# Performance work log

Measured on AMD Instinct MI355X. Metric: run time of the kernel, lower is better.

Reference implementation:

```python
import jax, jax.numpy as jnp
import numpy as np

B, T, N, IN_DIM = 32, 12, 1024, 1
HID, EMB, K, HOR, OUT = 64, 16, 2, 12, 1


def setup_inputs() -> dict:
    key = jax.random.key(0)
    ks = jax.random.split(key, 12)
    s = 0.1
    return {
        "x": jax.random.normal(ks[0], (B, T, N, IN_DIM), jnp.float32),
        "E": jax.random.normal(ks[1], (N, EMB), jnp.float32),
        # layer 1: gate (z,r) and candidate pools; in = IN_DIM + HID
        "Wg1": jax.random.normal(ks[2], (EMB, K, IN_DIM + HID, 2 * HID), jnp.float32) * s,
        "bg1": jax.random.normal(ks[3], (EMB, 2 * HID), jnp.float32) * s,
        "Wc1": jax.random.normal(ks[4], (EMB, K, IN_DIM + HID, HID), jnp.float32) * s,
        "bc1": jax.random.normal(ks[5], (EMB, HID), jnp.float32) * s,
        # layer 2: in = HID + HID
        "Wg2": jax.random.normal(ks[6], (EMB, K, 2 * HID, 2 * HID), jnp.float32) * s,
        "bg2": jax.random.normal(ks[7], (EMB, 2 * HID), jnp.float32) * s,
        "Wc2": jax.random.normal(ks[8], (EMB, K, 2 * HID, HID), jnp.float32) * s,
        "bc2": jax.random.normal(ks[9], (EMB, HID), jnp.float32) * s,
        # Conv2d(1, HOR*OUT, kernel=(1, HID)) == per-node linear HID -> HOR*OUT
        "Wout": jax.random.normal(ks[10], (HOR * OUT, HID), jnp.float32) * s,
        "bout": jnp.zeros((HOR * OUT,), jnp.float32),
    }


def _supports(E):
    # adaptive adjacency from node embeddings + Chebyshev polynomial set
    A = jax.nn.softmax(jax.nn.relu(E @ E.T), axis=1)  # [N, N]
    sup = [jnp.eye(E.shape[0], dtype=E.dtype), A]
    for _ in range(K - 2):
        sup.append(2.0 * (A @ sup[-1]) - sup[-2])
    return jnp.stack(sup[:K])  # [K, N, N]


def _gconv(x, sup, E, Wp, bp):
    # x: [B, N, Ci]; per-node weights generated from embeddings
    xg = jnp.einsum('knm,bmc->bnkc', sup, x)          # [B, N, K, Ci]
    W = jnp.einsum('nd,dkio->nkio', E, Wp)            # [N, K, Ci, Co]
    b = E @ bp                                        # [N, Co]
    return jnp.einsum('bnki,nkio->bno', xg, W) + b


def _layer(xs, sup, E, Wg, bg, Wc, bc):
    # xs: [T, B, N, Ci]; adaptive graph-conv GRU scanned over time
    hid = Wc.shape[-1]

    def step(h, x_t):
        zr = jax.nn.sigmoid(_gconv(jnp.concatenate([x_t, h], -1), sup, E, Wg, bg))
        z, r = jnp.split(zr, 2, axis=-1)
        hc = jnp.tanh(_gconv(jnp.concatenate([x_t, z * h], -1), sup, E, Wc, bc))
        h_new = r * h + (1.0 - r) * hc
        return h_new, h_new

    h0 = jnp.zeros((xs.shape[1], xs.shape[2], hid), xs.dtype)
    _, hs = jax.lax.scan(step, h0, xs)
    return hs  # [T, B, N, hid]


def reference(x, E, Wg1, bg1, Wc1, bc1, Wg2, bg2, Wc2, bc2, Wout, bout):
    sup = _supports(E)
    xs = jnp.swapaxes(x, 0, 1)                        # [T, B, N, in]
    h1 = _layer(xs, sup, E, Wg1, bg1, Wc1, bc1)       # [T, B, N, HID]
    h2 = _layer(h1, sup, E, Wg2, bg2, Wc2, bc2)       # [T, B, N, HID]
    h_last = h2[-1]                                   # [B, N, HID]
    out = jnp.einsum('bnh,oh->bno', h_last, Wout) + bout  # [B, N, HOR*OUT]
    out = jnp.transpose(out, (0, 2, 1)).reshape(x.shape[0], HOR, OUT, N)
    return jnp.transpose(out, (0, 1, 3, 2))           # [B, HOR, N, OUT]
```

## Files before the change

kernel.cpp:

```cpp
#include <hip/hip_runtime.h>
#include <math.h>

#define NN 1024
#define BB 32
#define TTT 12
#define HH 64
#define DD 16

__device__ __forceinline__ float dot4f(const float4 v, const float* __restrict__ wv) {
    return v.x * wv[0] + v.y * wv[1] + v.z * wv[2] + v.w * wv[3];
}

__device__ __forceinline__ float sigmoidf_(float x) { return 1.0f / (1.0f + expf(-x)); }

__global__ __launch_bounds__(256) void compute_A_kernel(const float* __restrict__ E,
                                                        float* __restrict__ A) {
    int n = blockIdx.x;
    int tid = threadIdx.x;
    __shared__ float en[DD];
    __shared__ float red[256];
    if (tid < DD) en[tid] = E[n * DD + tid];
    __syncthreads();
    float s[4];
    float lmax = 0.0f;
    #pragma unroll
    for (int it = 0; it < 4; ++it) {
        int m = tid + it * 256;
        float acc = 0.0f;
        #pragma unroll
        for (int d = 0; d < DD; ++d) acc += en[d] * E[m * DD + d];
        acc = fmaxf(acc, 0.0f);
        s[it] = acc;
        lmax = fmaxf(lmax, acc);
    }
    red[tid] = lmax; __syncthreads();
    for (int st = 128; st > 0; st >>= 1) {
        if (tid < st) red[tid] = fmaxf(red[tid], red[tid + st]);
        __syncthreads();
    }
    float mx = red[0];
    __syncthreads();
    float lsum = 0.0f;
    #pragma unroll
    for (int it = 0; it < 4; ++it) { s[it] = expf(s[it] - mx); lsum += s[it]; }
    red[tid] = lsum; __syncthreads();
    for (int st = 128; st > 0; st >>= 1) {
        if (tid < st) red[tid] += red[tid + st];
        __syncthreads();
    }
    float inv = 1.0f / red[0];
    #pragma unroll
    for (int it = 0; it < 4; ++it) {
        int m = tid + it * 256;
        A[n * NN + m] = s[it] * inv;
    }
}

__global__ __launch_bounds__(256) void gen_w_f32_kernel(const float* __restrict__ E,
                                                        const float* __restrict__ Wp,
                                                        float* __restrict__ out,
                                                        int rowlen, int total) {
    int idx = blockIdx.x * 256 + threadIdx.x;
    if (idx >= total) return;
    int n = idx / rowlen;
    int j = idx - n * rowlen;
    const float* e = E + n * DD;
    float acc = 0.0f;
    #pragma unroll
    for (int d = 0; d < DD; ++d) acc += e[d] * Wp[d * rowlen + j];
    out[idx] = acc;
}

__global__ __launch_bounds__(256) void gen_w4_kernel(const float* __restrict__ E,
                                                     const float4* __restrict__ Wp4,
                                                     float4* __restrict__ out4,
                                                     int rowlen4, int total4) {
    int idx = blockIdx.x * 256 + threadIdx.x;
    if (idx >= total4) return;
    int n = idx / rowlen4;
    int j = idx - n * rowlen4;
    const float* e = E + n * DD;
    float4 acc = make_float4(0.f, 0.f, 0.f, 0.f);
    #pragma unroll
    for (int d = 0; d < DD; ++d) {
        float ed = e[d];
        float4 w = Wp4[(size_t)d * rowlen4 + j];
        acc.x += ed * w.x; acc.y += ed * w.y; acc.z += ed * w.z; acc.w += ed * w.w;
    }
    out4[idx] = acc;
}

__global__ __launch_bounds__(256) void transpose_x_kernel(const float* __restrict__ x,
                                                          float* __restrict__ xTm) {
    int idx = blockIdx.x * 256 + threadIdx.x;
    int m = idx / (TTT * BB);
    int tb = idx - m * (TTT * BB);
    int t = tb >> 5;
    int b = tb & 31;
    xTm[idx] = x[(b * TTT + t) * NN + m];
}

__global__ __launch_bounds__(256) void diffuse_gemm(const float* __restrict__ A,
                                                    const float* __restrict__ S,
                                                    float* __restrict__ C, int cols) {
    __shared__ alignas(16) float As[2][16][68];
    __shared__ alignas(16) float Bs[2][16][64];
    const int tid = threadIdx.x;
    const int tx = tid & 15, ty = tid >> 4;
    const int rowbase = blockIdx.y * 64, colbase = blockIdx.x * 64;
    const int kl = tid & 15, r0 = (tid >> 4) * 4;
    const int ml = tid >> 6, cl = tid & 63;
    float pa[4], pb[4];
    #pragma unroll
    for (int r = 0; r < 4; ++r)
        pa[r] = A[(size_t)(rowbase + r0 + r) * NN + kl];
    #pragma unroll
    for (int mm = 0; mm < 4; ++mm)
        pb[mm] = S[(size_t)(ml + mm * 4) * cols + colbase + cl];
    #pragma unroll
    for (int r = 0; r < 4; ++r) As[0][kl][r0 + r] = pa[r];
    #pragma unroll
    for (int mm = 0; mm < 4; ++mm) Bs[0][ml + mm * 4][cl] = pb[mm];
    __syncthreads();
    int cur = 0;
    float acc[4][4] = {};
    for (int kt = 0; kt < NN; kt += 16) {
        int kn = kt + 16;
        if (kn < NN) {
            #pragma unroll
            for (int r = 0; r < 4; ++r)
                pa[r] = A[(size_t)(rowbase + r0 + r) * NN + kn + kl];
            #pragma unroll
            for (int mm = 0; mm < 4; ++mm)
                pb[mm] = S[(size_t)(kn + ml + mm * 4) * cols + colbase + cl];
        }
        #pragma unroll
        for (int kk = 0; kk < 16; ++kk) {
            float4 a = *(const float4*)&As[cur][kk][ty * 4];
            float4 b = *(const float4*)&Bs[cur][kk][tx * 4];
            acc[0][0] += a.x * b.x; acc[0][1] += a.x * b.y; acc[0][2] += a.x * b.z; acc[0][3] += a.x * b.w;
            acc[1][0] += a.y * b.x; acc[1][1] += a.y * b.y; acc[1][2] += a.y * b.z; acc[1][3] += a.y * b.w;
            acc[2][0] += a.z * b.x; acc[2][1] += a.z * b.y; acc[2][2] += a.z * b.z; acc[2][3] += a.z * b.w;
            acc[3][0] += a.w * b.x; acc[3][1] += a.w * b.y; acc[3][2] += a.w * b.z; acc[3][3] += a.w * b.w;
        }
        if (kn < NN) {
            int nxt = cur ^ 1;
            #pragma unroll
            for (int r = 0; r < 4; ++r) As[nxt][kl][r0 + r] = pa[r];
            #pragma unroll
            for (int mm = 0; mm < 4; ++mm) Bs[nxt][ml + mm * 4][cl] = pb[mm];
            __syncthreads();
            cur = nxt;
        }
    }
    #pragma unroll
    for (int i = 0; i < 4; ++i) {
        float4 v = make_float4(acc[i][0], acc[i][1], acc[i][2], acc[i][3]);
        *(float4*)&C[(size_t)(rowbase + ty * 4 + i) * cols + colbase + tx * 4] = v;
    }
}


__global__ __launch_bounds__(256) void l1_gate_kernel(int t,
        const float* __restrict__ xTm, const float* __restrict__ AxA,
        const float* __restrict__ h1, const float* __restrict__ Ah1,
        const float* __restrict__ Wg, const float* __restrict__ Bg,
        float* __restrict__ zh, float* __restrict__ rb) {
    int n = blockIdx.x;
    int tid = threadIdx.x;
    __shared__ alignas(16) float sh[BB * HH];
    __shared__ alignas(16) float sa[BB * HH];
    __shared__ float sx[BB], sax[BB];
    for (int i = tid; i < BB * HH; i += 256) {
        sh[i] = h1[(size_t)n * (BB * HH) + i];
        sa[i] = Ah1[(size_t)n * (BB * HH) + i];
    }
    if (tid < BB) sx[tid] = xTm[n * (TTT * BB) + t * BB + tid];
    else if (tid < 2 * BB) sax[tid - BB] = AxA[n * (TTT * BB) + t * BB + (tid - BB)];
    __syncthreads();
    const int o = tid & 63;
    const int bq = tid >> 6;
    const float* W = Wg + (size_t)n * 16640;
    float accA[8], accB[8];
    float biasA = Bg[n * 128 + o], biasB = Bg[n * 128 + 64 + o];
    float wxa0 = W[o], wxa1 = W[8320 + o];
    float wxb0 = W[64 + o], wxb1 = W[8320 + 64 + o];
    #pragma unroll
    for (int j = 0; j < 8; ++j) {
        int b = bq * 8 + j;
        accA[j] = biasA + sx[b] * wxa0 + sax[b] * wxa1;
        accB[j] = biasB + sx[b] * wxb0 + sax[b] * wxb1;
    }
    for (int i = 0; i < HH; i += 4) {
        float w0a[4], w1a[4], w0b[4], w1b[4];
        #pragma unroll
        for (int q = 0; q < 4; ++q) {
            int row = (1 + i + q) * 128;
            w0a[q] = W[row + o];            w1a[q] = W[8320 + row + o];
            w0b[q] = W[row + 64 + o];       w1b[q] = W[8320 + row + 64 + o];
        }
        #pragma unroll
        for (int j = 0; j < 8; ++j) {
            int b = bq * 8 + j;
            float4 hv = *(const float4*)&sh[b * HH + i];
            float4 av = *(const float4*)&sa[b * HH + i];
            accA[j] += dot4f(hv, w0a) + dot4f(av, w1a);
            accB[j] += dot4f(hv, w0b) + dot4f(av, w1b);
        }
    }
    #pragma unroll
    for (int j = 0; j < 8; ++j) {
        int b = bq * 8 + j;
        float z = sigmoidf_(accA[j]);
        float r = sigmoidf_(accB[j]);
        zh[(size_t)n * (BB * HH) + b * HH + o] = z * sh[b * HH + o];
        rb[(size_t)n * (BB * HH) + b * HH + o] = r;
    }
}

__global__ __launch_bounds__(256) void l1_cand_kernel(int t,
        const float* __restrict__ xTm, const float* __restrict__ AxA,
        const float* __restrict__ zhb, const float* __restrict__ azh,
        const float* __restrict__ Wc, const float* __restrict__ Bc,
        const float* __restrict__ rb, float* __restrict__ h1) {
    int n = blockIdx.x;
    int tid = threadIdx.x;
    __shared__ alignas(16) float sz[BB * HH];
    __shared__ alignas(16) float saz[BB * HH];
    __shared__ float sx[BB], sax[BB];
    for (int i = tid; i < BB * HH; i += 256) {
        sz[i] = zhb[(size_t)n * (BB * HH) + i];
        saz[i] = azh[(size_t)n * (BB * HH) + i];
    }
    if (tid < BB) sx[tid] = xTm[n * (TTT * BB) + t * BB + tid];
    else if (tid < 2 * BB) sax[tid - BB] = AxA[n * (TTT * BB) + t * BB + (tid - BB)];
    __syncthreads();
    const int o = tid & 63;
    const int bq = tid >> 6;
    const float* W = Wc + (size_t)n * 8320;
    float acc[8];
    float bias = Bc[n * 64 + o];
    float wx0 = W[o], wx1 = W[4160 + o];
    #pragma unroll
    for (int j = 0; j < 8; ++j) {
        int b = bq * 8 + j;
        acc[j] = bias + sx[b] * wx0 + sax[b] * wx1;
    }
    for (int i = 0; i < HH; i += 4) {
        float w0[4], w1[4];
        #pragma unroll
        for (int q = 0; q < 4; ++q) {
            int row = (1 + i + q) * 64;
            w0[q] = W[row + o];
            w1[q] = W[4160 + row + o];
        }
        #pragma unroll
        for (int j = 0; j < 8; ++j) {
            int b = bq * 8 + j;
            float4 zv = *(const float4*)&sz[b * HH + i];
            float4 av = *(const float4*)&saz[b * HH + i];
            acc[j] += dot4f(zv, w0) + dot4f(av, w1);
        }
    }
    #pragma unroll
    for (int j = 0; j < 8; ++j) {
        int b = bq * 8 + j;
        size_t idx = (size_t)n * (BB * HH) + b * HH + o;
        float hc = tanhf(acc[j]);
        float r = rb[idx];
        float hold = h1[idx];
        h1[idx] = r * hold + (1.0f - r) * hc;
    }
}


__global__ __launch_bounds__(256) void l2_gate_fused(
        const float* __restrict__ h1, const float* __restrict__ Ah1,
        const float* __restrict__ h2, const float* __restrict__ Ah2,
        const float* __restrict__ E, const float4* __restrict__ Wp4,
        const float* __restrict__ Bg,
        float* __restrict__ zh, float* __restrict__ rb) {
    int n = blockIdx.x, tid = threadIdx.x;
    __shared__ float en[DD];
    __shared__ alignas(16) float Wl[64 * 128];
    __shared__ alignas(16) float Sl[4][BB * HH];
    if (tid < DD) en[tid] = E[n * DD + tid];
    for (int i = tid; i < BB * HH; i += 256) {
        size_t base = (size_t)n * (BB * HH) + i;
        Sl[0][i] = h1[base]; Sl[1][i] = h2[base];
        Sl[2][i] = Ah1[base]; Sl[3][i] = Ah2[base];
    }
    __syncthreads();
    const int o = tid & 63, bq = tid >> 6;
    float accA[8], accB[8];
    float biasA = Bg[n * 128 + o], biasB = Bg[n * 128 + 64 + o];
    #pragma unroll
    for (int j = 0; j < 8; ++j) { accA[j] = biasA; accB[j] = biasB; }
    for (int p = 0; p < 4; ++p) {
        int k = p >> 1, half = p & 1;
        for (int idx = tid; idx < 2048; idx += 256) {
            float4 a = make_float4(0.f, 0.f, 0.f, 0.f);
            #pragma unroll
            for (int d = 0; d < DD; ++d) {
                float ed = en[d];
                float4 w = Wp4[(size_t)d * 8192 + k * 4096 + half * 2048 + idx];
                a.x += ed * w.x; a.y += ed * w.y; a.z += ed * w.z; a.w += ed * w.w;
            }
            *(float4*)&Wl[idx * 4] = a;
        }
        __syncthreads();
        const float* S = Sl[k * 2 + half];
        for (int i = 0; i < HH; i += 4) {
            float wa[4], wb[4];
            #pragma unroll
            for (int q = 0; q < 4; ++q) {
                int row = (i + q) * 128;
                wa[q] = Wl[row + o]; wb[q] = Wl[row + 64 + o];
            }
            #pragma unroll
            for (int j = 0; j < 8; ++j) {
                int b = bq * 8 + j;
                float4 sv = *(const float4*)&S[b * HH + i];
                accA[j] += dot4f(sv, wa); accB[j] += dot4f(sv, wb);
            }
        }
        __syncthreads();
    }
    #pragma unroll
    for (int j = 0; j < 8; ++j) {
        int b = bq * 8 + j;
        float z = sigmoidf_(accA[j]);
        float r = sigmoidf_(accB[j]);
        zh[(size_t)n * (BB * HH) + b * HH + o] = z * Sl[1][b * HH + o];
        rb[(size_t)n * (BB * HH) + b * HH + o] = r;
    }
}

__global__ __launch_bounds__(256) void l2_cand_fused(
        const float* __restrict__ h1, const float* __restrict__ Ah1,
        const float* __restrict__ zhb, const float* __restrict__ azh,
        const float* __restrict__ E, const float4* __restrict__ Wp4,
        const float* __restrict__ Bc,
        const float* __restrict__ rb, float* __restrict__ h2) {
    int n = blockIdx.x, tid = threadIdx.x;
    __shared__ float en[DD];
    __shared__ alignas(16) float Wl[64 * 64];
    __shared__ alignas(16) float Sl[4][BB * HH];
    if (tid < DD) en[tid] = E[n * DD + tid];
    for (int i = tid; i < BB * HH; i += 256) {
        size_t base = (size_t)n * (BB * HH) + i;
        Sl[0][i] = h1[base];  Sl[1][i] = zhb[base];
        Sl[2][i] = Ah1[base]; Sl[3][i] = azh[base];
    }
    __syncthreads();
    const int o = tid & 63, bq = tid >> 6;
    float acc[8];
    float bias = Bc[n * 64 + o];
    #pragma unroll
    for (int j = 0; j < 8; ++j) acc[j] = bias;
    for (int p = 0; p < 4; ++p) {
        int k = p >> 1, half = p & 1;
        for (int idx = tid; idx < 1024; idx += 256) {
            float4 a = make_float4(0.f, 0.f, 0.f, 0.f);
            #pragma unroll
            for (int d = 0; d < DD; ++d) {
                float ed = en[d];
                float4 w = Wp4[(size_t)d * 4096 + k * 2048 + half * 1024 + idx];
                a.x += ed * w.x; a.y += ed * w.y; a.z += ed * w.z; a.w += ed * w.w;
            }
            *(float4*)&Wl[idx * 4] = a;
        }
        __syncthreads();
        const float* S = Sl[k * 2 + half];
        for (int i = 0; i < HH; i += 4) {
            float wa[4];
            #pragma unroll
            for (int qq = 0; qq < 4; ++qq) wa[qq] = Wl[(i + qq) * 64 + o];
            #pragma unroll
            for (int j = 0; j < 8; ++j) {
                int b = bq * 8 + j;
                float4 sv = *(const float4*)&S[b * HH + i];
                acc[j] += dot4f(sv, wa);
            }
        }
        __syncthreads();
    }
    #pragma unroll
    for (int j = 0; j < 8; ++j) {
        int b = bq * 8 + j;
        size_t idx = (size_t)n * (BB * HH) + b * HH + o;
        float hc = tanhf(acc[j]);
        float r = rb[idx];
        float hold = h2[idx];
        h2[idx] = r * hold + (1.0f - r) * hc;
    }
}

__global__ __launch_bounds__(384) void out_kernel(const float* __restrict__ h2,
                                                  const float* __restrict__ Wout,
                                                  const float* __restrict__ bout,
                                                  float* __restrict__ out) {
    int n = blockIdx.x;
    int tid = threadIdx.x;
    __shared__ float shh[BB * HH];
    __shared__ float sw[TTT * HH];
    __shared__ float sb[TTT];
    for (int i = tid; i < BB * HH; i += 384) shh[i] = h2[(size_t)n * (BB * HH) + i];
    for (int i = tid; i < TTT * HH; i += 384) sw[i] = Wout[i];
    if (tid < TTT) sb[tid] = bout[tid];
    __syncthreads();
    int b = tid & 31;
    int hor = tid >> 5;
    float acc = sb[hor];
    #pragma unroll
    for (int c = 0; c < HH; ++c) acc += shh[b * HH + c] * sw[hor * HH + c];
    out[(size_t)(b * TTT + hor) * NN + n] = acc;
}

__global__ void report_ws_kernel(float* out, float v) { out[0] = v; }

extern "C" void kernel_launch(void* const* d_in, const int* in_sizes, int n_in,
                              void* d_out, int out_size, void* d_ws, size_t ws_size,
                              hipStream_t stream) {
    const float* x    = (const float*)d_in[0];
    const float* E    = (const float*)d_in[1];
    const float* Wg1p = (const float*)d_in[2];
    const float* bg1p = (const float*)d_in[3];
    const float* Wc1p = (const float*)d_in[4];
    const float* bc1p = (const float*)d_in[5];
    const float* Wg2p = (const float*)d_in[6];
    const float* bg2p = (const float*)d_in[7];
    const float* Wc2p = (const float*)d_in[8];
    const float* bc2p = (const float*)d_in[9];
    const float* Wout = (const float*)d_in[10];
    const float* bout = (const float*)d_in[11];
    float* out = (float*)d_out;
    float* ws = (float*)d_ws;

    size_t off = 0;
    float* A_   = ws + off; off += (size_t)NN * NN;
    float* B1g  = ws + off; off += (size_t)NN * 128;
    float* B1c  = ws + off; off += (size_t)NN * 64;
    float* B2g  = ws + off; off += (size_t)NN * 128;
    float* B2c  = ws + off; off += (size_t)NN * 64;
    float* xTm  = ws + off; off += (size_t)NN * TTT * BB;
    float* AxA  = ws + off; off += (size_t)NN * TTT * BB;
    const size_t ST = (size_t)NN * BB * HH;
    float* h1   = ws + off; off += ST;
    float* h2   = ws + off; off += ST;
    float* Ah1  = ws + off; off += ST;
    float* Ah2  = ws + off; off += ST;
    float* Azh  = ws + off; off += ST;
    float* ZH   = ws + off; off += ST;
    float* Rb   = ws + off; off += ST;
    float* W1G  = ws + off; off += (size_t)NN * 16640;
    float* W1C  = ws + off; off += (size_t)NN * 8320;
    size_t need_bytes = off * sizeof(float);
    if (ws_size < need_bytes) {
        report_ws_kernel<<<1, 1, 0, stream>>>(out, (float)ws_size);
        return;
    }

    (void)hipMemsetAsync(h1, 0, ST * 4, stream);
    (void)hipMemsetAsync(h2, 0, ST * 4, stream);
    (void)hipMemsetAsync(Ah1, 0, ST * 4, stream);
    (void)hipMemsetAsync(Ah2, 0, ST * 4, stream);
    (void)hipMemsetAsync(Azh, 0, ST * 4, stream);

    compute_A_kernel<<<NN, 256, 0, stream>>>(E, A_);
    gen_w_f32_kernel<<<(131072 + 255) / 256, 256, 0, stream>>>(E, bg1p, B1g, 128, 131072);
    gen_w_f32_kernel<<<(65536 + 255) / 256, 256, 0, stream>>>(E, bc1p, B1c, 64, 65536);
    gen_w_f32_kernel<<<(131072 + 255) / 256, 256, 0, stream>>>(E, bg2p, B2g, 128, 131072);
    gen_w_f32_kernel<<<(65536 + 255) / 256, 256, 0, stream>>>(E, bc2p, B2c, 64, 65536);
    transpose_x_kernel<<<(NN * TTT * BB) / 256, 256, 0, stream>>>(x, xTm);
    diffuse_gemm<<<dim3((TTT * BB) / 64, NN / 64), 256, 0, stream>>>(A_, xTm, AxA, TTT * BB);
    gen_w4_kernel<<<(4259840 + 255) / 256, 256, 0, stream>>>(
        E, (const float4*)Wg1p, (float4*)W1G, 4160, 4259840);
    gen_w4_kernel<<<(2129920 + 255) / 256, 256, 0, stream>>>(
        E, (const float4*)Wc1p, (float4*)W1C, 2080, 2129920);

    const int COLS = BB * HH;
    dim3 gemmGrid(COLS / 64, NN / 64);

    for (int t = 0; t < TTT; ++t) {
        l1_gate_kernel<<<NN, 256, 0, stream>>>(t, xTm, AxA, h1, Ah1, W1G, B1g, ZH, Rb);
        if (t > 0) diffuse_gemm<<<gemmGrid, 256, 0, stream>>>(A_, ZH, Azh, COLS);
        l1_cand_kernel<<<NN, 256, 0, stream>>>(t, xTm, AxA, ZH, Azh, W1C, B1c, Rb, h1);
        diffuse_gemm<<<gemmGrid, 256, 0, stream>>>(A_, h1, Ah1, COLS);
        l2_gate_fused<<<NN, 256, 0, stream>>>(h1, Ah1, h2, Ah2,
                                              E, (const float4*)Wg2p, B2g, ZH, Rb);
        if (t > 0) diffuse_gemm<<<gemmGrid, 256, 0, stream>>>(A_, ZH, Azh, COLS);
        l2_cand_fused<<<NN, 256, 0, stream>>>(h1, Ah1, ZH, Azh,
                                              E, (const float4*)Wc2p, B2c, Rb, h2);
        if (t < TTT - 1) diffuse_gemm<<<gemmGrid, 256, 0, stream>>>(A_, h2, Ah2, COLS);
    }

    out_kernel<<<NN, 384, 0, stream>>>(h2, Wout, bout, out);
}
```

Measured before the change: 6.200 ms.

## Stream layer-2 state slices through one shared buffer, prefetched during weight generation

The layer-2 gate and candidate kernels no longer stage all four state slices (32 KB) into shared memory up front. They keep a single 8 KB slice buffer and load each slice with float4 loads into registers before the per-node weight generation loop, so the loads overlap that compute before being written to shared memory. This cuts shared memory per block, which should allow more resident blocks per CU, and hides global load latency. In exchange the weight-generation loop is fully unrolled, which raises register use, and the gate epilogue now rereads h2 from global memory.

```diff
diff --git a/kernel.cpp b/kernel.cpp
--- a/kernel.cpp
+++ b/kernel.cpp
@@ -283,14 +283,10 @@
     int n = blockIdx.x, tid = threadIdx.x;
     __shared__ float en[DD];
     __shared__ alignas(16) float Wl[64 * 128];
-    __shared__ alignas(16) float Sl[4][BB * HH];
+    __shared__ alignas(16) float Sp[BB * HH];
     if (tid < DD) en[tid] = E[n * DD + tid];
-    for (int i = tid; i < BB * HH; i += 256) {
-        size_t base = (size_t)n * (BB * HH) + i;
-        Sl[0][i] = h1[base]; Sl[1][i] = h2[base];
-        Sl[2][i] = Ah1[base]; Sl[3][i] = Ah2[base];
-    }
-    __syncthreads();
+    __syncthreads();
+    const float* states[4] = {h1, h2, Ah1, Ah2};
     const int o = tid & 63, bq = tid >> 6;
     float accA[8], accB[8];
     float biasA = Bg[n * 128 + o], biasB = Bg[n * 128 + 64 + o];
@@ -298,7 +294,11 @@
     for (int j = 0; j < 8; ++j) { accA[j] = biasA; accB[j] = biasB; }
     for (int p = 0; p < 4; ++p) {
         int k = p >> 1, half = p & 1;
-        for (int idx = tid; idx < 2048; idx += 256) {
+        const float4* Sg = (const float4*)(states[p] + (size_t)n * (BB * HH));
+        float4 s0 = Sg[tid], s1 = Sg[tid + 256];
+        #pragma unroll
+        for (int it = 0; it < 8; ++it) {
+            int idx = tid + it * 256;
             float4 a = make_float4(0.f, 0.f, 0.f, 0.f);
             #pragma unroll
             for (int d = 0; d < DD; ++d) {
@@ -306,10 +306,11 @@
                 float4 w = Wp4[(size_t)d * 8192 + k * 4096 + half * 2048 + idx];
                 a.x += ed * w.x; a.y += ed * w.y; a.z += ed * w.z; a.w += ed * w.w;
             }
-            *(float4*)&Wl[idx * 4] = a;
-        }
+            ((float4*)Wl)[idx] = a;
+        }
+        ((float4*)Sp)[tid] = s0;
+        ((float4*)Sp)[tid + 256] = s1;
         __syncthreads();
-        const float* S = Sl[k * 2 + half];
         for (int i = 0; i < HH; i += 4) {
             float wa[4], wb[4];
             #pragma unroll
@@ -320,7 +321,7 @@
             #pragma unroll
             for (int j = 0; j < 8; ++j) {
                 int b = bq * 8 + j;
-                float4 sv = *(const float4*)&S[b * HH + i];
+                float4 sv = *(const float4*)&Sp[b * HH + i];
                 accA[j] += dot4f(sv, wa); accB[j] += dot4f(sv, wb);
             }
         }
@@ -331,8 +332,9 @@
         int b = bq * 8 + j;
         float z = sigmoidf_(accA[j]);
         float r = sigmoidf_(accB[j]);
-        zh[(size_t)n * (BB * HH) + b * HH + o] = z * Sl[1][b * HH + o];
-        rb[(size_t)n * (BB * HH) + b * HH + o] = r;
+        size_t idx = (size_t)n * (BB * HH) + b * HH + o;
+        zh[idx] = z * h2[idx];
+        rb[idx] = r;
     }
 }
 
@@ -345,14 +347,10 @@
     int n = blockIdx.x, tid = threadIdx.x;
     __shared__ float en[DD];
     __shared__ alignas(16) float Wl[64 * 64];
-    __shared__ alignas(16) float Sl[4][BB * HH];
+    __shared__ alignas(16) float Sp[BB * HH];
     if (tid < DD) en[tid] = E[n * DD + tid];
-    for (int i = tid; i < BB * HH; i += 256) {
-        size_t base = (size_t)n * (BB * HH) + i;
-        Sl[0][i] = h1[base];  Sl[1][i] = zhb[base];
-        Sl[2][i] = Ah1[base]; Sl[3][i] = azh[base];
-    }
-    __syncthreads();
+    __syncthreads();
+    const float* states[4] = {h1, zhb, Ah1, azh};
     const int o = tid & 63, bq = tid >> 6;
     float acc[8];
     float bias = Bc[n * 64 + o];
@@ -360,7 +358,11 @@
     for (int j = 0; j < 8; ++j) acc[j] = bias;
     for (int p = 0; p < 4; ++p) {
         int k = p >> 1, half = p & 1;
-        for (int idx = tid; idx < 1024; idx += 256) {
+        const float4* Sg = (const float4*)(states[p] + (size_t)n * (BB * HH));
+        float4 s0 = Sg[tid], s1 = Sg[tid + 256];
+        #pragma unroll
+        for (int it = 0; it < 4; ++it) {
+            int idx = tid + it * 256;
             float4 a = make_float4(0.f, 0.f, 0.f, 0.f);
             #pragma unroll
             for (int d = 0; d < DD; ++d) {
@@ -368,10 +370,11 @@
                 float4 w = Wp4[(size_t)d * 4096 + k * 2048 + half * 1024 + idx];
                 a.x += ed * w.x; a.y += ed * w.y; a.z += ed * w.z; a.w += ed * w.w;
             }
-            *(float4*)&Wl[idx * 4] = a;
-        }
+            ((float4*)Wl)[idx] = a;
+        }
+        ((float4*)Sp)[tid] = s0;
+        ((float4*)Sp)[tid + 256] = s1;
         __syncthreads();
-        const float* S = Sl[k * 2 + half];
         for (int i = 0; i < HH; i += 4) {
             float wa[4];
             #pragma unroll
@@ -379,7 +382,7 @@
             #pragma unroll
             for (int j = 0; j < 8; ++j) {
                 int b = bq * 8 + j;
-                float4 sv = *(const float4*)&S[b * HH + i];
+                float4 sv = *(const float4*)&Sp[b * HH + i];
                 acc[j] += dot4f(sv, wa);
             }
         }
```

New measurement: 6.785 ms. 9.4% more time.
